# Performance work log

Hardware: AMD Instinct MI355X
Metric: run time of the kernel (lower is better)

## Reference

```python
import jax, jax.numpy as jnp
import numpy as np

K = 7     # kernel_size
H_HEADS = 16  # h


def setup_inputs() -> dict:
    key = jax.random.key(0)
    k1, k2 = jax.random.split(key)
    B, S, D = 8, 2048, 1024
    x = jax.random.normal(k1, (B, S, D), dtype=jnp.float32)
    W = jax.random.normal(k2, (D, K * H_HEADS), dtype=jnp.float32) * (1.0 / np.sqrt(D))
    b = jnp.zeros((K * H_HEADS,), dtype=jnp.float32)
    return {"x": x, "W": W, "b": b}


def reference(x, W, b):
    B, S, D = x.shape
    L = S - K + 1  # number of output positions
    rep = D // H_HEADS
    # dynamic kernels from positions K-1..S-1: [B, L, K, h]
    kern = (x[:, K - 1:] @ W + b).reshape(B, L, K, H_HEADS)
    kern = jax.nn.softmax(kern, axis=-2)
    # tf.tile([1,1,1,rep]): repeat the whole h-block rep times -> [B, L, K, D]
    kern = jnp.tile(kern, (1, 1, 1, rep))
    # sliding windows: windows[b, i, k] = x[b, i + k]  -> [B, L, K, D]
    idx = jnp.arange(L)[:, None] + jnp.arange(K)[None, :]
    windows = x[:, idx]
    # weighted mean over the kernel axis (tf.reduce_mean)
    out = jnp.mean(kern * windows, axis=2)  # [B, L, D]
    return out
```

## Files before the change

kernel.cpp:

```cpp
#include <hip/hip_runtime.h>


#define KK 7
#define HH 16
#define DD 1024
#define SS 2048
#define LL 2042
#define NO 112
#define TL 16
#define WTF_BYTES (7 * 32 * 64 * 8 * 2)

typedef __attribute__((ext_vector_type(8))) short bf16x8;
typedef __attribute__((ext_vector_type(4))) float f32x4;

__device__ __forceinline__ unsigned short f2bf(float f) {
    unsigned u = __builtin_bit_cast(unsigned, f);
    u += 0x7fffu + ((u >> 16) & 1u);
    return (unsigned short)(u >> 16);
}
__device__ __forceinline__ unsigned bfpack(float lo, float hi) {
    return (unsigned)f2bf(lo) | ((unsigned)f2bf(hi) << 16);
}
__device__ __forceinline__ float bflo(unsigned u) {
    return __builtin_bit_cast(float, u << 16);
}
__device__ __forceinline__ float bfhi(unsigned u) {
    return __builtin_bit_cast(float, u & 0xffff0000u);
}

__global__ void wprep(const float* __restrict__ W, unsigned short* __restrict__ wtf) {
    const int bx = blockIdx.x;
    const int lane = threadIdx.x;
    const int i = bx >> 5, ks = bx & 31;
    const int frow = lane & 15, fq = lane >> 4;
    const int col = i * 16 + frow;
    const int k0 = ks * 32 + fq * 8;
    unsigned p[4];
#pragma unroll
    for (int j = 0; j < 4; ++j) {
        float a = W[(size_t)(k0 + 2 * j) * NO + col];
        float b = W[(size_t)(k0 + 2 * j + 1) * NO + col];
        p[j] = bfpack(a, b);
    }
    *(uint4*)(wtf + (size_t)(bx * 64 + lane) * 8) = make_uint4(p[0], p[1], p[2], p[3]);
}

template <bool WSOK>
__global__ __launch_bounds__(512, 8)
void dlconv(const float* __restrict__ x, const float* __restrict__ W,
            const float* __restrict__ bias, const unsigned short* __restrict__ wtf,
            float* __restrict__ out)
{
    __shared__ __align__(16) unsigned char smem[40192];
    float* Lg = (float*)(smem + 32768);
    const int t  = threadIdx.x;
    const int lb = blockIdx.x, b = blockIdx.y;
    const int l0 = lb * TL;
    const float* xb = x + (size_t)b * SS * DD;

#pragma unroll
    for (int s = 0; s < 8; ++s) {
        int idx = t + 512 * s;
        int row = idx >> 8, c4 = idx & 255;
        int gr = l0 + 6 + row; gr = gr < SS ? gr : SS - 1;
        float4 v = *(const float4*)(xb + (size_t)gr * DD + c4 * 4);
        int addr = row * 2048 + ((c4 * 8) ^ ((row & 7) << 4));
        *(uint2*)(smem + addr) = make_uint2(bfpack(v.x, v.y), bfpack(v.z, v.w));
    }
    __syncthreads();

    const int lane = t & 63, wid = t >> 6;
    const int frow = lane & 15, fq = lane >> 4;
    if (wid < 7) {
        const int abase = frow * 2048;
        const int aswz = (frow & 7) << 4;
        f32x4 acc = (f32x4)0.f;
#pragma unroll 8
        for (int ks = 0; ks < 32; ++ks) {
            bf16x8 af = *(const bf16x8*)(smem + abase + ((ks * 64 + fq * 16) ^ aswz));
            bf16x8 bf;
            if constexpr (WSOK) {
                bf = *(const bf16x8*)(wtf + (size_t)((wid * 32 + ks) * 64 + lane) * 8);
            } else {
                const float* wp = W + (size_t)(ks * 32 + fq * 8) * NO + wid * 16 + frow;
                short e0 = (short)f2bf(wp[0 * NO]), e1 = (short)f2bf(wp[1 * NO]);
                short e2 = (short)f2bf(wp[2 * NO]), e3 = (short)f2bf(wp[3 * NO]);
                short e4 = (short)f2bf(wp[4 * NO]), e5 = (short)f2bf(wp[5 * NO]);
                short e6 = (short)f2bf(wp[6 * NO]), e7 = (short)f2bf(wp[7 * NO]);
                bf = bf16x8{e0, e1, e2, e3, e4, e5, e6, e7};
            }
            acc = __builtin_amdgcn_mfma_f32_16x16x32_bf16(af, bf, acc, 0, 0, 0);
        }
        float bi = bias[wid * 16 + frow];
#pragma unroll
        for (int reg = 0; reg < 4; ++reg)
            Lg[(fq * 4 + reg) * 116 + wid * 16 + frow] = acc[reg] + bi;
    }
    __syncthreads();

    if (t < 256) {
        const int r = t >> 4, h = t & 15;
        float v[KK];
        float m = -1e30f;
#pragma unroll
        for (int i = 0; i < KK; ++i) {
            v[i] = Lg[r * 116 + i * 16 + h];
            m = fmaxf(m, v[i]);
        }
        float ssum = 0.f;
#pragma unroll
        for (int i = 0; i < KK; ++i) { v[i] = __expf(v[i] - m); ssum += v[i]; }
        float inv = 1.f / (7.f * ssum);
#pragma unroll
        for (int i = 0; i < KK; ++i) Lg[r * 116 + i * 16 + h] = v[i] * inv;
    }
    __syncthreads();

    const int rg = t >> 8;
    const int cc = t & 255;
    const int hs = (cc & 3) << 2;
    const int coff = cc * 8;
    float* orow0 = out + ((size_t)b * LL + l0) * DD + cc * 4;

    if (rg == 0) {
        f32x4 gx[6];
#pragma unroll
        for (int j = 0; j < 6; ++j)
            gx[j] = *(const f32x4*)(xb + (size_t)(l0 + j) * DD + cc * 4);
#pragma unroll
        for (int q = 0; q < 8; ++q) {
            f32x4 o = (f32x4)0.f;
#pragma unroll
            for (int k = 0; k < KK; ++k) {
                f32x4 pv = *(const f32x4*)(Lg + q * 116 + k * 16 + hs);
                if (q + k < 6) {
                    o += pv * gx[q + k];
                } else {
                    int rr = q + k - 6;
                    uint2 u = *(const uint2*)(smem + rr * 2048 + (coff ^ ((rr & 7) << 4)));
                    f32x4 xv = { bflo(u.x), bfhi(u.x), bflo(u.y), bfhi(u.y) };
                    o += pv * xv;
                }
            }
            *(f32x4*)(orow0 + (size_t)q * DD) = o;
        }
    } else {
#pragma unroll
        for (int q = 0; q < 8; ++q) {
            int row = 8 + q;
            if (l0 + row < LL) {
                f32x4 o = (f32x4)0.f;
#pragma unroll
                for (int k = 0; k < KK; ++k) {
                    int rr = row + k - 6;
                    f32x4 pv = *(const f32x4*)(Lg + row * 116 + k * 16 + hs);
                    uint2 u = *(const uint2*)(smem + rr * 2048 + (coff ^ ((rr & 7) << 4)));
                    f32x4 xv = { bflo(u.x), bfhi(u.x), bflo(u.y), bfhi(u.y) };
                    o += pv * xv;
                }
                *(f32x4*)(orow0 + (size_t)row * DD) = o;
            }
        }
    }
}

extern "C" void kernel_launch(void* const* d_in, const int* in_sizes, int n_in,
                              void* d_out, int out_size, void* d_ws, size_t ws_size,
                              hipStream_t stream) {
    const float* x    = (const float*)d_in[0];
    const float* W    = (const float*)d_in[1];
    const float* bias = (const float*)d_in[2];
    float* out        = (float*)d_out;
    dim3 grid((LL + TL - 1) / TL, 8);
    const bool wsok = (ws_size >= (size_t)WTF_BYTES) && d_ws != nullptr;
    if (wsok) {
        unsigned short* wtf = (unsigned short*)d_ws;
        wprep<<<224, 64, 0, stream>>>(W, wtf);
        dlconv<true><<<grid, 512, 0, stream>>>(x, W, bias, wtf, out);
    } else {
        dlconv<false><<<grid, 512, 0, stream>>>(x, W, bias, nullptr, out);
    }
}
```

Measured before the change: 36.35 us.

## Halve row tile to 8 with 256-thread blocks and batch-interleaved block order

Shrinks each block to 8 output rows and 256 threads, so 4 waves cover the 7 logit column tiles (3 waves do two MFMA chains) and MFMA rows 8-15 duplicate the 8 valid rows. Block indices are remapped so consecutive blocks walk across batches. Each thread now computes one output row group directly from global x for the halo rows. The aim is more, smaller blocks for better occupancy and load balance, at the cost of more redundant halo loads (6 of every 14 rows) and wasted MFMA work.

```diff
diff --git a/kernel.cpp b/kernel.cpp
--- a/kernel.cpp
+++ b/kernel.cpp
@@ -7,7 +7,7 @@
 #define SS 2048
 #define LL 2042
 #define NO 112
-#define TL 16
+#define TL 8
 #define WTF_BYTES (7 * 32 * 64 * 8 * 2)
 
 typedef __attribute__((ext_vector_type(8))) short bf16x8;
@@ -46,59 +46,79 @@
 }
 
 template <bool WSOK>
-__global__ __launch_bounds__(512, 8)
+__global__ __launch_bounds__(256, 8)
 void dlconv(const float* __restrict__ x, const float* __restrict__ W,
             const float* __restrict__ bias, const unsigned short* __restrict__ wtf,
             float* __restrict__ out)
 {
-    __shared__ __align__(16) unsigned char smem[40192];
-    float* Lg = (float*)(smem + 32768);
-    const int t  = threadIdx.x;
-    const int lb = blockIdx.x, b = blockIdx.y;
+    __shared__ __align__(16) unsigned char smem[20096];
+    float* Lg = (float*)(smem + 16384);
+    const int t = threadIdx.x;
+
+    const int flat = blockIdx.x + (blockIdx.y << 8);
+    const int n = ((flat & 7) << 8) + (flat >> 3);
+    const int lb = n & 255, b = n >> 8;
     const int l0 = lb * TL;
     const float* xb = x + (size_t)b * SS * DD;
 
 #pragma unroll
     for (int s = 0; s < 8; ++s) {
-        int idx = t + 512 * s;
+        int idx = t + 256 * s;
         int row = idx >> 8, c4 = idx & 255;
         int gr = l0 + 6 + row; gr = gr < SS ? gr : SS - 1;
         float4 v = *(const float4*)(xb + (size_t)gr * DD + c4 * 4);
-        int addr = row * 2048 + ((c4 * 8) ^ ((row & 7) << 4));
+        int addr = row * 2048 + ((c4 * 8) ^ (row << 4));
         *(uint2*)(smem + addr) = make_uint2(bfpack(v.x, v.y), bfpack(v.z, v.w));
     }
     __syncthreads();
 
     const int lane = t & 63, wid = t >> 6;
     const int frow = lane & 15, fq = lane >> 4;
-    if (wid < 7) {
-        const int abase = frow * 2048;
-        const int aswz = (frow & 7) << 4;
-        f32x4 acc = (f32x4)0.f;
+    {
+        const int ar = frow & 7;
+        const int abase = ar * 2048;
+        const int aswz = ar << 4;
+        f32x4 acc0 = (f32x4)0.f, acc1 = (f32x4)0.f;
 #pragma unroll 8
         for (int ks = 0; ks < 32; ++ks) {
             bf16x8 af = *(const bf16x8*)(smem + abase + ((ks * 64 + fq * 16) ^ aswz));
-            bf16x8 bf;
             if constexpr (WSOK) {
-                bf = *(const bf16x8*)(wtf + (size_t)((wid * 32 + ks) * 64 + lane) * 8);
+                bf16x8 b0 = *(const bf16x8*)(wtf + (size_t)((wid * 32 + ks) * 64 + lane) * 8);
+                acc0 = __builtin_amdgcn_mfma_f32_16x16x32_bf16(af, b0, acc0, 0, 0, 0);
+                if (wid < 3) {
+                    bf16x8 b1 = *(const bf16x8*)(wtf + (size_t)(((wid + 4) * 32 + ks) * 64 + lane) * 8);
+                    acc1 = __builtin_amdgcn_mfma_f32_16x16x32_bf16(af, b1, acc1, 0, 0, 0);
+                }
             } else {
-                const float* wp = W + (size_t)(ks * 32 + fq * 8) * NO + wid * 16 + frow;
-                short e0 = (short)f2bf(wp[0 * NO]), e1 = (short)f2bf(wp[1 * NO]);
-                short e2 = (short)f2bf(wp[2 * NO]), e3 = (short)f2bf(wp[3 * NO]);
-                short e4 = (short)f2bf(wp[4 * NO]), e5 = (short)f2bf(wp[5 * NO]);
-                short e6 = (short)f2bf(wp[6 * NO]), e7 = (short)f2bf(wp[7 * NO]);
-                bf = bf16x8{e0, e1, e2, e3, e4, e5, e6, e7};
+                const float* wp0 = W + (size_t)(ks * 32 + fq * 8) * NO + wid * 16 + frow;
+                bf16x8 b0 = bf16x8{(short)f2bf(wp0[0 * NO]), (short)f2bf(wp0[1 * NO]),
+                                   (short)f2bf(wp0[2 * NO]), (short)f2bf(wp0[3 * NO]),
+                                   (short)f2bf(wp0[4 * NO]), (short)f2bf(wp0[5 * NO]),
+                                   (short)f2bf(wp0[6 * NO]), (short)f2bf(wp0[7 * NO])};
+                acc0 = __builtin_amdgcn_mfma_f32_16x16x32_bf16(af, b0, acc0, 0, 0, 0);
+                if (wid < 3) {
+                    const float* wp1 = wp0 + 64;
+                    bf16x8 b1 = bf16x8{(short)f2bf(wp1[0 * NO]), (short)f2bf(wp1[1 * NO]),
+                                       (short)f2bf(wp1[2 * NO]), (short)f2bf(wp1[3 * NO]),
+                                       (short)f2bf(wp1[4 * NO]), (short)f2bf(wp1[5 * NO]),
+                                       (short)f2bf(wp1[6 * NO]), (short)f2bf(wp1[7 * NO])};
+                    acc1 = __builtin_amdgcn_mfma_f32_16x16x32_bf16(af, b1, acc1, 0, 0, 0);
+                }
             }
-            acc = __builtin_amdgcn_mfma_f32_16x16x32_bf16(af, bf, acc, 0, 0, 0);
         }
-        float bi = bias[wid * 16 + frow];
+        if (fq < 2) {
 #pragma unroll
-        for (int reg = 0; reg < 4; ++reg)
-            Lg[(fq * 4 + reg) * 116 + wid * 16 + frow] = acc[reg] + bi;
+            for (int reg = 0; reg < 4; ++reg) {
+                int r = fq * 4 + reg;
+                Lg[r * 116 + wid * 16 + frow] = acc0[reg] + bias[wid * 16 + frow];
+                if (wid < 3)
+                    Lg[r * 116 + (wid + 4) * 16 + frow] = acc1[reg] + bias[(wid + 4) * 16 + frow];
+            }
+        }
     }
     __syncthreads();
 
-    if (t < 256) {
+    if (t < 128) {
         const int r = t >> 4, h = t & 15;
         float v[KK];
         float m = -1e30f;
@@ -116,50 +136,28 @@
     }
     __syncthreads();
 
-    const int rg = t >> 8;
-    const int cc = t & 255;
+    const int cc = t;
     const int hs = (cc & 3) << 2;
     const int coff = cc * 8;
     float* orow0 = out + ((size_t)b * LL + l0) * DD + cc * 4;
-
-    if (rg == 0) {
-        f32x4 gx[6];
 #pragma unroll
-        for (int j = 0; j < 6; ++j)
-            gx[j] = *(const f32x4*)(xb + (size_t)(l0 + j) * DD + cc * 4);
-#pragma unroll
-        for (int q = 0; q < 8; ++q) {
+    for (int q = 0; q < 8; ++q) {
+        if (l0 + q < LL) {
             f32x4 o = (f32x4)0.f;
 #pragma unroll
             for (int k = 0; k < KK; ++k) {
                 f32x4 pv = *(const f32x4*)(Lg + q * 116 + k * 16 + hs);
                 if (q + k < 6) {
-                    o += pv * gx[q + k];
+                    f32x4 g = *(const f32x4*)(xb + (size_t)(l0 + q + k) * DD + cc * 4);
+                    o += pv * g;
                 } else {
                     int rr = q + k - 6;
-                    uint2 u = *(const uint2*)(smem + rr * 2048 + (coff ^ ((rr & 7) << 4)));
+                    uint2 u = *(const uint2*)(smem + rr * 2048 + (coff ^ (rr << 4)));
                     f32x4 xv = { bflo(u.x), bfhi(u.x), bflo(u.y), bfhi(u.y) };
                     o += pv * xv;
                 }
             }
             *(f32x4*)(orow0 + (size_t)q * DD) = o;
-        }
-    } else {
-#pragma unroll
-        for (int q = 0; q < 8; ++q) {
-            int row = 8 + q;
-            if (l0 + row < LL) {
-                f32x4 o = (f32x4)0.f;
-#pragma unroll
-                for (int k = 0; k < KK; ++k) {
-                    int rr = row + k - 6;
-                    f32x4 pv = *(const f32x4*)(Lg + row * 116 + k * 16 + hs);
-                    uint2 u = *(const uint2*)(smem + rr * 2048 + (coff ^ ((rr & 7) << 4)));
-                    f32x4 xv = { bflo(u.x), bfhi(u.x), bflo(u.y), bfhi(u.y) };
-                    o += pv * xv;
-                }
-                *(f32x4*)(orow0 + (size_t)row * DD) = o;
-            }
         }
     }
 }
@@ -171,13 +169,13 @@
     const float* W    = (const float*)d_in[1];
     const float* bias = (const float*)d_in[2];
     float* out        = (float*)d_out;
-    dim3 grid((LL + TL - 1) / TL, 8);
+    dim3 grid(256, 8);
     const bool wsok = (ws_size >= (size_t)WTF_BYTES) && d_ws != nullptr;
     if (wsok) {
         unsigned short* wtf = (unsigned short*)d_ws;
         wprep<<<224, 64, 0, stream>>>(W, wtf);
-        dlconv<true><<<grid, 512, 0, stream>>>(x, W, bias, wtf, out);
+        dlconv<true><<<grid, 256, 0, stream>>>(x, W, bias, wtf, out);
     } else {
-        dlconv<false><<<grid, 512, 0, stream>>>(x, W, bias, nullptr, out);
+        dlconv<false><<<grid, 256, 0, stream>>>(x, W, bias, nullptr, out);
     }
 }
```

New measurement: 52.47 us. +44.4%, slower.
